# Performance work log

Hardware: AMD Instinct MI355X
Metric: run time of the kernel (lower is better)

The kernel has to match this reference:

```python
import jax, jax.numpy as jnp
import numpy as np

N_NODES = 100000


def gcn_conv(x, W, b, src, dst, n_nodes):
    # x: [N, Fin], W: [Fin, Fout], edge (src->dst) with self-loops added,
    # symmetric normalization D^{-1/2} A D^{-1/2} as in PyG GCNConv defaults.
    h = x @ W  # [N, Fout]
    loops = jnp.arange(n_nodes, dtype=src.dtype)
    src_all = jnp.concatenate([src, loops])
    dst_all = jnp.concatenate([dst, loops])
    ones = jnp.ones(src_all.shape[0], dtype=h.dtype)
    deg = jax.ops.segment_sum(ones, dst_all, num_segments=n_nodes)  # in-degree incl. self-loop
    dinv = jnp.where(deg > 0, jax.lax.rsqrt(deg), 0.0)
    norm = dinv[src_all] * dinv[dst_all]  # [E+N]
    msg = h[src_all] * norm[:, None]      # gather + scale
    out = jax.ops.segment_sum(msg, dst_all, num_segments=n_nodes)  # scatter-add
    return out + b


def setup_inputs() -> dict:
    key = jax.random.key(0)
    k1, k2, k3, k4 = jax.random.split(key, 4)
    in_dim, hidden, out_dim = 128, 128, 64
    n_edges = 600000
    x = jax.random.normal(k1, (N_NODES, in_dim), dtype=jnp.float32)
    edge_index = jax.random.randint(k2, (2, n_edges), 0, N_NODES, dtype=jnp.int64)
    # Glorot-ish init for weights
    W1 = jax.random.normal(k3, (in_dim, hidden), dtype=jnp.float32) / np.sqrt(in_dim)
    b1 = jnp.zeros((hidden,), dtype=jnp.float32)
    W2 = jax.random.normal(k4, (hidden, out_dim), dtype=jnp.float32) / np.sqrt(hidden)
    b2 = jnp.zeros((out_dim,), dtype=jnp.float32)
    return {"x": x, "edge_index": edge_index, "W1": W1, "b1": b1, "W2": W2, "b2": b2}


def reference(x, edge_index, W1, b1, W2, b2):
    src, dst = edge_index[0], edge_index[1]
    h = jax.nn.relu(gcn_conv(x, W1, b1, src, dst, N_NODES))
    # dropout is identity in eval mode (training=False)
    return gcn_conv(h, W2, b2, src, dst, N_NODES)
```

## Files before the change

### kernel.cpp

```cpp
#include <hip/hip_runtime.h>
#include <hip/hip_bf16.h>
#include <stdint.h>

typedef unsigned int u32;
typedef unsigned short u16;
typedef __attribute__((ext_vector_type(8))) short short8;
typedef __attribute__((ext_vector_type(4))) float f32x4;

#define SCAN_TILE 2048

__device__ __forceinline__ float bf2f(u16 u) {
    union { u32 u; float f; } v; v.u = ((u32)u) << 16; return v.f;
}
__device__ __forceinline__ u16 f2bf(float f) {
    u32 u = __float_as_uint(f);
    u32 r = (u + 0x7FFFu + ((u >> 16) & 1u)) >> 16;
    return (u16)r;
}
__device__ __forceinline__ u32 packbf(float lo, float hi) {
    return ((u32)f2bf(hi) << 16) | (u32)f2bf(lo);
}

__global__ __launch_bounds__(256) void detect_k(const u32* __restrict__ xw,
                                                const u32* __restrict__ ew,
                                                int* __restrict__ flags) {
    __shared__ int cnt;
    __shared__ u32 orr;
    int t = threadIdx.x;
    if (t == 0) { cnt = 0; orr = 0u; }
    __syncthreads();
    int hits = 0;
    for (int i = t; i < 1024; i += 256) {
        u32 f = (xw[i] >> 7) & 0xFFu;
        if (f >= 100u && f <= 140u) hits++;
    }
    atomicAdd(&cnt, hits);
    atomicOr(&orr, ew[2 * t + 1]);
    __syncthreads();
    if (t == 0) {
        flags[0] = (cnt < 512) ? 1 : 0;
        flags[1] = (orr == 0u) ? 1 : 0;
    }
}

template<int N>
__global__ __launch_bounds__(256) void w_pack_k(const void* __restrict__ W,
                                                uint4* __restrict__ wpk,
                                                const int* __restrict__ flags) {
    const int p = blockIdx.x * 256 + threadIdx.x;
    if (p >= 16 * N) return;
    const int n = p & (N - 1);
    const int kb = p >> ((N == 128) ? 7 : 6);
    u32 pk[4];
    if (flags[0]) {
        const float* wp = (const float*)W + (size_t)(kb * 8) * N + n;
        #pragma unroll
        for (int jj = 0; jj < 4; jj++)
            pk[jj] = packbf(wp[(2 * jj) * N], wp[(2 * jj + 1) * N]);
    } else {
        const u16* wp = (const u16*)W + (size_t)(kb * 8) * N + n;
        #pragma unroll
        for (int jj = 0; jj < 4; jj++)
            pk[jj] = ((u32)wp[(2 * jj + 1) * N] << 16) | (u32)wp[(2 * jj) * N];
    }
    uint4 v; v.x = pk[0]; v.y = pk[1]; v.z = pk[2]; v.w = pk[3];
    wpk[p] = v;
}

__global__ __launch_bounds__(256) void count_deg_k(const void* __restrict__ ei, int E,
                                                   const int* __restrict__ flags,
                                                   int* __restrict__ deg) {
    int i = blockIdx.x * 256 + threadIdx.x;
    if (i >= E) return;
    int d = flags[1] ? (int)((const long long*)ei)[E + i] : ((const int*)ei)[E + i];
    atomicAdd(&deg[d], 1);
}

__global__ __launch_bounds__(256) void scan_partial_k(const int* __restrict__ deg, int M,
                                                      int* __restrict__ bsum) {
    const int t = threadIdx.x;
    const int base = blockIdx.x * SCAN_TILE + t * 8;
    int s = 0;
    if (base + 8 <= M) {
        int4 a = *(const int4*)(deg + base);
        int4 b = *(const int4*)(deg + base + 4);
        s = a.x + a.y + a.z + a.w + b.x + b.y + b.z + b.w;
    } else {
        for (int j = 0; j < 8; j++) if (base + j < M) s += deg[base + j];
    }
    __shared__ int red[256];
    red[t] = s;
    __syncthreads();
    for (int d = 128; d > 0; d >>= 1) {
        if (t < d) red[t] += red[t + d];
        __syncthreads();
    }
    if (t == 0) bsum[blockIdx.x] = red[0];
}

__global__ __launch_bounds__(256) void scan_bsum_k(int* __restrict__ bsum, int nb,
                                                   int* __restrict__ off, int M) {
    __shared__ int buf[2][256];
    const int t = threadIdx.x;
    int v = (t < nb) ? bsum[t] : 0;
    const int own = v;
    buf[0][t] = v;
    __syncthreads();
    int cur = 0;
    for (int d = 1; d < 256; d <<= 1) {
        int x = buf[cur][t];
        if (t >= d) x += buf[cur][t - d];
        buf[cur ^ 1][t] = x;
        __syncthreads();
        cur ^= 1;
    }
    if (t < nb) bsum[t] = buf[cur][t] - own;
    if (t == 255) off[M] = buf[cur][255];
}

__global__ __launch_bounds__(256) void scan_final_k(const int* __restrict__ deg,
                                                    const int* __restrict__ bsum, int M,
                                                    int* __restrict__ off,
                                                    int* __restrict__ cursor,
                                                    float* __restrict__ dinv) {
    const int t = threadIdx.x;
    const int base = blockIdx.x * SCAN_TILE + t * 8;
    int v[8];
    int s = 0;
    const bool full = (base + 8 <= M);
    if (full) {
        int4 a = *(const int4*)(deg + base);
        int4 b = *(const int4*)(deg + base + 4);
        v[0] = a.x; v[1] = a.y; v[2] = a.z; v[3] = a.w;
        v[4] = b.x; v[5] = b.y; v[6] = b.z; v[7] = b.w;
        s = v[0] + v[1] + v[2] + v[3] + v[4] + v[5] + v[6] + v[7];
    } else {
        #pragma unroll
        for (int j = 0; j < 8; j++) { v[j] = (base + j < M) ? deg[base + j] : 0; s += v[j]; }
    }
    __shared__ int buf[2][256];
    buf[0][t] = s;
    __syncthreads();
    int cur = 0;
    for (int d = 1; d < 256; d <<= 1) {
        int x = buf[cur][t];
        if (t >= d) x += buf[cur][t - d];
        buf[cur ^ 1][t] = x;
        __syncthreads();
        cur ^= 1;
    }
    int pre = bsum[blockIdx.x] + buf[cur][t] - s;
    int o[8]; float dv[8];
    #pragma unroll
    for (int j = 0; j < 8; j++) {
        o[j] = pre;
        dv[j] = rsqrtf((float)(v[j] + 1));
        pre += v[j];
    }
    if (full) {
        *(int4*)(off + base)     = make_int4(o[0], o[1], o[2], o[3]);
        *(int4*)(off + base + 4) = make_int4(o[4], o[5], o[6], o[7]);
        *(int4*)(cursor + base)     = make_int4(o[0], o[1], o[2], o[3]);
        *(int4*)(cursor + base + 4) = make_int4(o[4], o[5], o[6], o[7]);
        *(float4*)(dinv + base)     = make_float4(dv[0], dv[1], dv[2], dv[3]);
        *(float4*)(dinv + base + 4) = make_float4(dv[4], dv[5], dv[6], dv[7]);
    } else {
        for (int j = 0; j < 8; j++) if (base + j < M) {
            off[base + j] = o[j]; cursor[base + j] = o[j]; dinv[base + j] = dv[j];
        }
    }
}

__global__ __launch_bounds__(256) void fill_k(const void* __restrict__ ei, int E,
                                              const int* __restrict__ flags,
                                              int* __restrict__ cursor, int* __restrict__ eidx) {
    int i = blockIdx.x * 256 + threadIdx.x;
    if (i >= E) return;
    int s, d;
    if (flags[1]) { const long long* p = (const long long*)ei; s = (int)p[i]; d = (int)p[E + i]; }
    else          { const int* p = (const int*)ei;             s = p[i];      d = p[E + i]; }
    int pos = atomicAdd(&cursor[d], 1);
    eidx[pos] = s;
}

template<int N>
__global__ __launch_bounds__(256) void gemm_mfma_k(
    const void* __restrict__ X, const uint4* __restrict__ wpk,
    const float* __restrict__ dinv, u16* __restrict__ HS,
    const int* __restrict__ flags, int x_is_ext, int M)
{
    constexpr int NT = N / 16;
    constexpr int NC8 = N / 8;
    __shared__ u32 xlds[128 * 64];
    const int t = threadIdx.x;
    const int wave = t >> 6, lane = t & 63;
    const int q = lane >> 4, m = lane & 15;
    const bool xf32 = (x_is_ext != 0) && (flags[0] != 0);
    const int row0 = blockIdx.x * 128;

    for (int c = t; c < 2048; c += 256) {
        const int row = c >> 4, c8 = c & 15;
        const int grow = row0 + row;
        uint4 pk = make_uint4(0u, 0u, 0u, 0u);
        if (grow < M) {
            if (xf32) {
                const float* xp = (const float*)X + (size_t)grow * 128 + c8 * 8;
                float4 u = *(const float4*)xp;
                float4 v = *(const float4*)(xp + 4);
                pk.x = packbf(u.x, u.y); pk.y = packbf(u.z, u.w);
                pk.z = packbf(v.x, v.y); pk.w = packbf(v.z, v.w);
            } else {
                pk = *(const uint4*)((const u16*)X + (size_t)grow * 128 + c8 * 8);
            }
        }
        *(uint4*)&xlds[row * 64 + c8 * 4] = pk;
    }
    __syncthreads();

    union { uint4 u; short8 v; } a[2][4];
    #pragma unroll
    for (int rt = 0; rt < 2; rt++)
        #pragma unroll
        for (int s = 0; s < 4; s++)
            a[rt][s].u = *(const uint4*)&xlds[(wave * 32 + rt * 16 + m) * 64 + (s * 4 + q) * 4];

    f32x4 acc[2][NT];
    #pragma unroll
    for (int rt = 0; rt < 2; rt++)
        #pragma unroll
        for (int tt = 0; tt < NT; tt++)
            acc[rt][tt] = (f32x4){0.f, 0.f, 0.f, 0.f};

    #pragma unroll
    for (int s = 0; s < 4; s++) {
        union { uint4 u; short8 v; } b[NT];
        #pragma unroll
        for (int tt = 0; tt < NT; tt++)
            b[tt].u = wpk[(s * 4 + q) * N + tt * 16 + m];
        #pragma unroll
        for (int tt = 0; tt < NT; tt++)
            #pragma unroll
            for (int rt = 0; rt < 2; rt++)
                acc[rt][tt] = __builtin_amdgcn_mfma_f32_16x16x32_bf16(
                    a[rt][s].v, b[tt].v, acc[rt][tt], 0, 0, 0);
    }

    float dv[2][4];
    #pragma unroll
    for (int rt = 0; rt < 2; rt++)
        #pragma unroll
        for (int r = 0; r < 4; r++) {
            const int grow = row0 + wave * 32 + rt * 16 + q * 4 + r;
            dv[rt][r] = (grow < M) ? dinv[grow] : 0.f;
        }

    u16* orow = (u16*)&xlds[wave * 32 * 64];
    #pragma unroll
    for (int rt = 0; rt < 2; rt++)
        #pragma unroll
        for (int tt = 0; tt < NT; tt++)
            #pragma unroll
            for (int r = 0; r < 4; r++)
                orow[(rt * 16 + q * 4 + r) * N + tt * 16 + m] =
                    f2bf(acc[rt][tt][r] * dv[rt][r]);

    constexpr int ITER = 16 * NC8 / 64;
    #pragma unroll
    for (int rt = 0; rt < 2; rt++) {
        #pragma unroll
        for (int j = 0; j < ITER; j++) {
            const int cc = lane + j * 64;
            const int lrow = cc / NC8, c8 = cc % NC8;
            const int grow = row0 + wave * 32 + rt * 16 + lrow;
            uint4 v = *(const uint4*)&((const u32*)orow)[(rt * 16 + lrow) * (N / 2) + c8 * 4];
            if (grow < M)
                *(uint4*)(HS + (size_t)grow * N + c8 * 8) = v;
        }
    }
}

template<int N, bool RELU>
__global__ __launch_bounds__(256) void aggregate_k(
    const u16* __restrict__ hs, const int* __restrict__ eidx,
    const int* __restrict__ off, const float* __restrict__ dinv,
    const void* __restrict__ bias, void* __restrict__ out,
    const int* __restrict__ flags, int out_is_ext, int M)
{
    constexpr int TPN = N / 8;
    constexpr int NPB = 256 / TPN;
    const int node = blockIdx.x * NPB + threadIdx.x / TPN;
    const int lane = threadIdx.x % TPN;
    if (node >= M) return;
    const int f32io = flags[0];
    const int beg = off[node], end = off[node + 1];
    const int c8 = lane * 8;
    const u16* __restrict__ hrow = hs + c8;

    float a[8];
    {
        uint4 sp = *(const uint4*)(hrow + (size_t)node * N);
        const u16* s = (const u16*)&sp;
        #pragma unroll
        for (int j = 0; j < 8; j++) a[j] = bf2f(s[j]);
    }

    int p = beg;
    for (; p + 4 <= end; p += 4) {
        const int s0 = eidx[p + 0], s1 = eidx[p + 1];
        const int s2 = eidx[p + 2], s3 = eidx[p + 3];
        uint4 v0 = *(const uint4*)(hrow + (size_t)s0 * N);
        uint4 v1 = *(const uint4*)(hrow + (size_t)s1 * N);
        uint4 v2 = *(const uint4*)(hrow + (size_t)s2 * N);
        uint4 v3 = *(const uint4*)(hrow + (size_t)s3 * N);
        const u16* q0 = (const u16*)&v0; const u16* q1 = (const u16*)&v1;
        const u16* q2 = (const u16*)&v2; const u16* q3 = (const u16*)&v3;
        #pragma unroll
        for (int j = 0; j < 8; j++)
            a[j] += (bf2f(q0[j]) + bf2f(q1[j])) + (bf2f(q2[j]) + bf2f(q3[j]));
    }
    for (; p < end; p++) {
        const int s = eidx[p];
        uint4 v = *(const uint4*)(hrow + (size_t)s * N);
        const u16* q = (const u16*)&v;
        #pragma unroll
        for (int j = 0; j < 8; j++) a[j] += bf2f(q[j]);
    }

    const float dv = dinv[node];
    float b[8];
    if (f32io) {
        float4 u = *(const float4*)((const float*)bias + c8);
        float4 v = *(const float4*)((const float*)bias + c8 + 4);
        b[0] = u.x; b[1] = u.y; b[2] = u.z; b[3] = u.w;
        b[4] = v.x; b[5] = v.y; b[6] = v.z; b[7] = v.w;
    } else {
        uint4 u = *(const uint4*)((const u16*)bias + c8);
        const u16* s = (const u16*)&u;
        #pragma unroll
        for (int j = 0; j < 8; j++) b[j] = bf2f(s[j]);
    }
    float o[8];
    #pragma unroll
    for (int j = 0; j < 8; j++) {
        o[j] = fmaf(dv, a[j], b[j]);
        if (RELU) o[j] = fmaxf(o[j], 0.f);
    }
    if (out_is_ext && f32io) {
        float* op = (float*)out + (size_t)node * N + c8;
        *(float4*)op       = make_float4(o[0], o[1], o[2], o[3]);
        *(float4*)(op + 4) = make_float4(o[4], o[5], o[6], o[7]);
    } else {
        uint4 pk;
        pk.x = packbf(o[0], o[1]); pk.y = packbf(o[2], o[3]);
        pk.z = packbf(o[4], o[5]); pk.w = packbf(o[6], o[7]);
        *(uint4*)((u16*)out + (size_t)node * N + c8) = pk;
    }
}

extern "C" void kernel_launch(void* const* d_in, const int* in_sizes, int n_in,
                              void* d_out, int out_size, void* d_ws, size_t ws_size,
                              hipStream_t stream) {
    const void* x  = d_in[0];
    const void* ei = d_in[1];
    const void* W1 = d_in[2];
    const void* b1 = d_in[3];
    const void* W2 = d_in[4];
    const void* b2 = d_in[5];

    const int M = in_sizes[0] / 128;
    const int E = in_sizes[1] / 2;
    const int NB = (M + SCAN_TILE - 1) / SCAN_TILE;

    char* ws = (char*)d_ws;
    size_t offb = 0;
    auto alloc = [&](size_t bytes) -> void* {
        void* p = ws + offb; offb += (bytes + 255) & ~(size_t)255; return p;
    };
    int*   flags  = (int*)  alloc(256);
    int*   bsum   = (int*)  alloc(1024);
    uint4* wpk1   = (uint4*)alloc(16 * 128 * 16);
    uint4* wpk2   = (uint4*)alloc(16 * 64 * 16);
    int*   deg    = (int*)  alloc((size_t)M * 4);
    int*   off    = (int*)  alloc((size_t)(M + 1) * 4);
    int*   cursor = (int*)  alloc((size_t)M * 4);
    float* dinv   = (float*)alloc((size_t)M * 4);
    int*   eidx   = (int*)  alloc((size_t)E * 4);
    u16*   hs1    = (u16*)  alloc((size_t)M * 128 * 2);
    u16*   out1   = (u16*)  alloc((size_t)M * 128 * 2);
    u16*   hs2    = hs1;
    (void)ws_size; (void)n_in; (void)out_size;

    detect_k<<<1, 256, 0, stream>>>((const u32*)x, (const u32*)ei, flags);
    w_pack_k<128><<<8, 256, 0, stream>>>(W1, wpk1, flags);
    w_pack_k<64><<<4, 256, 0, stream>>>(W2, wpk2, flags);

    hipMemsetAsync(deg, 0, (size_t)M * 4, stream);
    count_deg_k<<<(E + 255) / 256, 256, 0, stream>>>(ei, E, flags, deg);
    scan_partial_k<<<NB, 256, 0, stream>>>(deg, M, bsum);
    scan_bsum_k<<<1, 256, 0, stream>>>(bsum, NB, off, M);
    scan_final_k<<<NB, 256, 0, stream>>>(deg, bsum, M, off, cursor, dinv);
    fill_k<<<(E + 255) / 256, 256, 0, stream>>>(ei, E, flags, cursor, eidx);

    gemm_mfma_k<128><<<(M + 127) / 128, 256, 0, stream>>>(x, wpk1, dinv, hs1, flags, 1, M);
    aggregate_k<128, true><<<(M + 15) / 16, 256, 0, stream>>>(hs1, eidx, off, dinv, b1, out1,
                                                              flags, 0, M);
    gemm_mfma_k<64><<<(M + 127) / 128, 256, 0, stream>>>(out1, wpk2, dinv, hs2, flags, 0, M);
    aggregate_k<64, false><<<(M + 31) / 32, 256, 0, stream>>>(hs2, eidx, off, dinv, b2, d_out,
                                                              flags, 1, M);
}
```

Before: 248.3 us.

## Fuse layer-1 aggregation with layer-2 GEMM and merge small setup kernels

Layer-1 neighbor aggregation (bias and ReLU included) now runs in the same kernel as the layer-2 MFMA GEMM. The aggregated 128-row tile is staged in LDS instead of being written to and reread from a global intermediate buffer. The deg memset is folded into the detection kernel, and the two weight-pack kernels are merged into one launch, cutting launch count. The cost is a 32KB LDS tile per block and only 8 iterations of 16 nodes per block, which lowers occupancy and the latency hiding available to the irregular gathers.

```diff
diff --git a/kernel.cpp b/kernel.cpp
--- a/kernel.cpp
+++ b/kernel.cpp
@@ -21,38 +21,41 @@
     return ((u32)f2bf(hi) << 16) | (u32)f2bf(lo);
 }
 
-__global__ __launch_bounds__(256) void detect_k(const u32* __restrict__ xw,
-                                                const u32* __restrict__ ew,
-                                                int* __restrict__ flags) {
-    __shared__ int cnt;
-    __shared__ u32 orr;
-    int t = threadIdx.x;
-    if (t == 0) { cnt = 0; orr = 0u; }
-    __syncthreads();
-    int hits = 0;
-    for (int i = t; i < 1024; i += 256) {
-        u32 f = (xw[i] >> 7) & 0xFFu;
-        if (f >= 100u && f <= 140u) hits++;
-    }
-    atomicAdd(&cnt, hits);
-    atomicOr(&orr, ew[2 * t + 1]);
-    __syncthreads();
-    if (t == 0) {
-        flags[0] = (cnt < 512) ? 1 : 0;
-        flags[1] = (orr == 0u) ? 1 : 0;
+__global__ __launch_bounds__(256) void detect_zero_k(const u32* __restrict__ xw,
+                                                     const u32* __restrict__ ew,
+                                                     int* __restrict__ flags,
+                                                     int* __restrict__ deg, int M) {
+    const int t = threadIdx.x;
+    const int i4 = (blockIdx.x * 256 + t) * 4;
+    if (i4 + 4 <= M) *(int4*)(deg + i4) = make_int4(0, 0, 0, 0);
+    else { for (int j = 0; j < 4; j++) if (i4 + j < M) deg[i4 + j] = 0; }
+
+    if (blockIdx.x == 0) {
+        __shared__ int cnt;
+        __shared__ u32 orr;
+        if (t == 0) { cnt = 0; orr = 0u; }
+        __syncthreads();
+        int hits = 0;
+        for (int i = t; i < 1024; i += 256) {
+            u32 f = (xw[i] >> 7) & 0xFFu;
+            if (f >= 100u && f <= 140u) hits++;
+        }
+        atomicAdd(&cnt, hits);
+        atomicOr(&orr, ew[2 * t + 1]);
+        __syncthreads();
+        if (t == 0) {
+            flags[0] = (cnt < 512) ? 1 : 0;
+            flags[1] = (orr == 0u) ? 1 : 0;
+        }
     }
 }
 
 template<int N>
-__global__ __launch_bounds__(256) void w_pack_k(const void* __restrict__ W,
-                                                uint4* __restrict__ wpk,
-                                                const int* __restrict__ flags) {
-    const int p = blockIdx.x * 256 + threadIdx.x;
-    if (p >= 16 * N) return;
+__device__ __forceinline__ void wpack_one(const void* W, uint4* wpk, int p, int f32w) {
     const int n = p & (N - 1);
     const int kb = p >> ((N == 128) ? 7 : 6);
     u32 pk[4];
-    if (flags[0]) {
+    if (f32w) {
         const float* wp = (const float*)W + (size_t)(kb * 8) * N + n;
         #pragma unroll
         for (int jj = 0; jj < 4; jj++)
@@ -65,6 +68,17 @@
     }
     uint4 v; v.x = pk[0]; v.y = pk[1]; v.z = pk[2]; v.w = pk[3];
     wpk[p] = v;
+}
+
+__global__ __launch_bounds__(256) void wpack_all_k(const void* __restrict__ W1,
+                                                   const void* __restrict__ W2,
+                                                   uint4* __restrict__ wpk1,
+                                                   uint4* __restrict__ wpk2,
+                                                   const int* __restrict__ flags) {
+    const int b = blockIdx.x, t = threadIdx.x;
+    const int f32w = flags[0];
+    if (b < 8) wpack_one<128>(W1, wpk1, b * 256 + t, f32w);
+    else       wpack_one<64> (W2, wpk2, (b - 8) * 256 + t, f32w);
 }
 
 __global__ __launch_bounds__(256) void count_deg_k(const void* __restrict__ ei, int E,
@@ -279,6 +293,140 @@
     }
 }
 
+__global__ __launch_bounds__(256) void agg_gemm_k(
+    const u16* __restrict__ hs, const int* __restrict__ eidx,
+    const int* __restrict__ off, const float* __restrict__ dinv,
+    const void* __restrict__ bias, const uint4* __restrict__ wpk2,
+    u16* __restrict__ HS2, const int* __restrict__ flags, int M)
+{
+    __shared__ u32 zlds[128 * 64];
+    const int t = threadIdx.x;
+    const int wave = t >> 6, lane = t & 63;
+    const int q = lane >> 4, m = lane & 15;
+    const int row0 = blockIdx.x * 128;
+    const int f32io = flags[0];
+    const int l16 = t & 15, c8 = l16 * 8;
+    const u16* __restrict__ hrow = hs + c8;
+
+    float b[8];
+    if (f32io) {
+        float4 u = *(const float4*)((const float*)bias + c8);
+        float4 v = *(const float4*)((const float*)bias + c8 + 4);
+        b[0] = u.x; b[1] = u.y; b[2] = u.z; b[3] = u.w;
+        b[4] = v.x; b[5] = v.y; b[6] = v.z; b[7] = v.w;
+    } else {
+        uint4 u = *(const uint4*)((const u16*)bias + c8);
+        const u16* s = (const u16*)&u;
+        #pragma unroll
+        for (int j = 0; j < 8; j++) b[j] = bf2f(s[j]);
+    }
+
+    for (int it = 0; it < 8; it++) {
+        const int lr = it * 16 + (t >> 4);
+        const int node = row0 + lr;
+        uint4 zpk = make_uint4(0u, 0u, 0u, 0u);
+        if (node < M) {
+            float a[8];
+            {
+                uint4 sp = *(const uint4*)(hrow + (size_t)node * 128);
+                const u16* s = (const u16*)&sp;
+                #pragma unroll
+                for (int j = 0; j < 8; j++) a[j] = bf2f(s[j]);
+            }
+            const int beg = off[node], end = off[node + 1];
+            int p = beg;
+            for (; p + 4 <= end; p += 4) {
+                const int s0 = eidx[p + 0], s1 = eidx[p + 1];
+                const int s2 = eidx[p + 2], s3 = eidx[p + 3];
+                uint4 v0 = *(const uint4*)(hrow + (size_t)s0 * 128);
+                uint4 v1 = *(const uint4*)(hrow + (size_t)s1 * 128);
+                uint4 v2 = *(const uint4*)(hrow + (size_t)s2 * 128);
+                uint4 v3 = *(const uint4*)(hrow + (size_t)s3 * 128);
+                const u16* q0 = (const u16*)&v0; const u16* q1 = (const u16*)&v1;
+                const u16* q2 = (const u16*)&v2; const u16* q3 = (const u16*)&v3;
+                #pragma unroll
+                for (int j = 0; j < 8; j++)
+                    a[j] += (bf2f(q0[j]) + bf2f(q1[j])) + (bf2f(q2[j]) + bf2f(q3[j]));
+            }
+            for (; p < end; p++) {
+                const int s = eidx[p];
+                uint4 v = *(const uint4*)(hrow + (size_t)s * 128);
+                const u16* qq = (const u16*)&v;
+                #pragma unroll
+                for (int j = 0; j < 8; j++) a[j] += bf2f(qq[j]);
+            }
+            const float dv = dinv[node];
+            float z[8];
+            #pragma unroll
+            for (int j = 0; j < 8; j++) z[j] = fmaxf(fmaf(dv, a[j], b[j]), 0.f);
+            zpk.x = packbf(z[0], z[1]); zpk.y = packbf(z[2], z[3]);
+            zpk.z = packbf(z[4], z[5]); zpk.w = packbf(z[6], z[7]);
+        }
+        *(uint4*)&zlds[lr * 64 + l16 * 4] = zpk;
+    }
+    __syncthreads();
+
+    union { uint4 u; short8 v; } a[2][4];
+    #pragma unroll
+    for (int rt = 0; rt < 2; rt++)
+        #pragma unroll
+        for (int s = 0; s < 4; s++)
+            a[rt][s].u = *(const uint4*)&zlds[(wave * 32 + rt * 16 + m) * 64 + (s * 4 + q) * 4];
+
+    f32x4 acc[2][4];
+    #pragma unroll
+    for (int rt = 0; rt < 2; rt++)
+        #pragma unroll
+        for (int tt = 0; tt < 4; tt++)
+            acc[rt][tt] = (f32x4){0.f, 0.f, 0.f, 0.f};
+
+    #pragma unroll
+    for (int s = 0; s < 4; s++) {
+        union { uint4 u; short8 v; } bb[4];
+        #pragma unroll
+        for (int tt = 0; tt < 4; tt++)
+            bb[tt].u = wpk2[(s * 4 + q) * 64 + tt * 16 + m];
+        #pragma unroll
+        for (int tt = 0; tt < 4; tt++)
+            #pragma unroll
+            for (int rt = 0; rt < 2; rt++)
+                acc[rt][tt] = __builtin_amdgcn_mfma_f32_16x16x32_bf16(
+                    a[rt][s].v, bb[tt].v, acc[rt][tt], 0, 0, 0);
+    }
+
+    float dv2[2][4];
+    #pragma unroll
+    for (int rt = 0; rt < 2; rt++)
+        #pragma unroll
+        for (int r = 0; r < 4; r++) {
+            const int grow = row0 + wave * 32 + rt * 16 + q * 4 + r;
+            dv2[rt][r] = (grow < M) ? dinv[grow] : 0.f;
+        }
+
+    u16* orow = (u16*)&zlds[wave * 32 * 64];
+    #pragma unroll
+    for (int rt = 0; rt < 2; rt++)
+        #pragma unroll
+        for (int tt = 0; tt < 4; tt++)
+            #pragma unroll
+            for (int r = 0; r < 4; r++)
+                orow[(rt * 16 + q * 4 + r) * 64 + tt * 16 + m] =
+                    f2bf(acc[rt][tt][r] * dv2[rt][r]);
+
+    #pragma unroll
+    for (int rt = 0; rt < 2; rt++) {
+        #pragma unroll
+        for (int j = 0; j < 2; j++) {
+            const int cc = lane + j * 64;
+            const int lrow = cc >> 3, c = cc & 7;
+            const int grow = row0 + wave * 32 + rt * 16 + lrow;
+            uint4 v = *(const uint4*)&((const u32*)orow)[(rt * 16 + lrow) * 32 + c * 4];
+            if (grow < M)
+                *(uint4*)(HS2 + (size_t)grow * 64 + c * 8) = v;
+        }
+    }
+}
+
 template<int N, bool RELU>
 __global__ __launch_bounds__(256) void aggregate_k(
     const u16* __restrict__ hs, const int* __restrict__ eidx,
@@ -386,15 +534,12 @@
     float* dinv   = (float*)alloc((size_t)M * 4);
     int*   eidx   = (int*)  alloc((size_t)E * 4);
     u16*   hs1    = (u16*)  alloc((size_t)M * 128 * 2);
-    u16*   out1   = (u16*)  alloc((size_t)M * 128 * 2);
-    u16*   hs2    = hs1;
+    u16*   hs2    = (u16*)  alloc((size_t)M * 64 * 2);
     (void)ws_size; (void)n_in; (void)out_size;
 
-    detect_k<<<1, 256, 0, stream>>>((const u32*)x, (const u32*)ei, flags);
-    w_pack_k<128><<<8, 256, 0, stream>>>(W1, wpk1, flags);
-    w_pack_k<64><<<4, 256, 0, stream>>>(W2, wpk2, flags);
-
-    hipMemsetAsync(deg, 0, (size_t)M * 4, stream);
+    detect_zero_k<<<(M + 1023) / 1024, 256, 0, stream>>>((const u32*)x, (const u32*)ei,
+                                                         flags, deg, M);
+    wpack_all_k<<<12, 256, 0, stream>>>(W1, W2, wpk1, wpk2, flags);
     count_deg_k<<<(E + 255) / 256, 256, 0, stream>>>(ei, E, flags, deg);
     scan_partial_k<<<NB, 256, 0, stream>>>(deg, M, bsum);
     scan_bsum_k<<<1, 256, 0, stream>>>(bsum, NB, off, M);
@@ -402,9 +547,8 @@
     fill_k<<<(E + 255) / 256, 256, 0, stream>>>(ei, E, flags, cursor, eidx);
 
     gemm_mfma_k<128><<<(M + 127) / 128, 256, 0, stream>>>(x, wpk1, dinv, hs1, flags, 1, M);
-    aggregate_k<128, true><<<(M + 15) / 16, 256, 0, stream>>>(hs1, eidx, off, dinv, b1, out1,
-                                                              flags, 0, M);
-    gemm_mfma_k<64><<<(M + 127) / 128, 256, 0, stream>>>(out1, wpk2, dinv, hs2, flags, 0, M);
+    agg_gemm_k<<<(M + 127) / 128, 256, 0, stream>>>(hs1, eidx, off, dinv, b1, wpk2, hs2,
+                                                    flags, M);
     aggregate_k<64, false><<<(M + 31) / 32, 256, 0, stream>>>(hs2, eidx, off, dinv, b2, d_out,
                                                               flags, 1, M);
 }
```

Measured after the change: 250.7 us. No clear change (+1.0%).

## Fuse CSR build into one persistent kernel with software grid barriers

Applied to the files above, without the earlier changes.

Replaces the detect, weight-pack, memset, degree-count, three-stage scan and fill kernels with two launches. The first zeroes degrees and detects flags. The second is a persistent 256-block kernel that packs weights, counts degrees, scans and fills edge indices, with atomic grid barriers between phases. The aim is to cut per-launch overhead and the idle gaps between the many small preprocessing kernels. The cost is spin-wait barriers, which depend on all 256 blocks being resident at once, and fewer threads for the atomic-heavy edge phases. hs2 now gets its own buffer instead of aliasing hs1.

```diff
diff --git a/kernel.cpp b/kernel.cpp
--- a/kernel.cpp
+++ b/kernel.cpp
@@ -7,7 +7,7 @@
 typedef __attribute__((ext_vector_type(8))) short short8;
 typedef __attribute__((ext_vector_type(4))) float f32x4;
 
-#define SCAN_TILE 2048
+#define CSRB 256
 
 __device__ __forceinline__ float bf2f(u16 u) {
     union { u32 u; float f; } v; v.u = ((u32)u) << 16; return v.f;
@@ -21,38 +21,60 @@
     return ((u32)f2bf(hi) << 16) | (u32)f2bf(lo);
 }
 
-__global__ __launch_bounds__(256) void detect_k(const u32* __restrict__ xw,
-                                                const u32* __restrict__ ew,
-                                                int* __restrict__ flags) {
-    __shared__ int cnt;
-    __shared__ u32 orr;
-    int t = threadIdx.x;
-    if (t == 0) { cnt = 0; orr = 0u; }
+__device__ __forceinline__ void grid_bar(int* cnt, int* gen, int nb) {
     __syncthreads();
-    int hits = 0;
-    for (int i = t; i < 1024; i += 256) {
-        u32 f = (xw[i] >> 7) & 0xFFu;
-        if (f >= 100u && f <= 140u) hits++;
-    }
-    atomicAdd(&cnt, hits);
-    atomicOr(&orr, ew[2 * t + 1]);
+    if (threadIdx.x == 0) {
+        __threadfence();
+        int g = __hip_atomic_load(gen, __ATOMIC_RELAXED, __HIP_MEMORY_SCOPE_AGENT);
+        int prev = __hip_atomic_fetch_add(cnt, 1, __ATOMIC_ACQ_REL, __HIP_MEMORY_SCOPE_AGENT);
+        if (prev == nb - 1) {
+            __hip_atomic_store(cnt, 0, __ATOMIC_RELAXED, __HIP_MEMORY_SCOPE_AGENT);
+            __hip_atomic_store(gen, g + 1, __ATOMIC_RELEASE, __HIP_MEMORY_SCOPE_AGENT);
+        } else {
+            while (__hip_atomic_load(gen, __ATOMIC_ACQUIRE, __HIP_MEMORY_SCOPE_AGENT) <= g)
+                __builtin_amdgcn_s_sleep(1);
+        }
+    }
     __syncthreads();
-    if (t == 0) {
-        flags[0] = (cnt < 512) ? 1 : 0;
-        flags[1] = (orr == 0u) ? 1 : 0;
+}
+
+__global__ __launch_bounds__(256) void detect_zero_k(const u32* __restrict__ xw,
+                                                     const u32* __restrict__ ew,
+                                                     int* __restrict__ flags,
+                                                     int* __restrict__ deg, int M) {
+    const int t = threadIdx.x;
+    const int i4 = (blockIdx.x * 256 + t) * 4;
+    if (i4 + 4 <= M) *(int4*)(deg + i4) = make_int4(0, 0, 0, 0);
+    else { for (int j = 0; j < 4; j++) if (i4 + j < M) deg[i4 + j] = 0; }
+
+    if (blockIdx.x == 0) {
+        __shared__ int cnt;
+        __shared__ u32 orr;
+        if (t == 0) { cnt = 0; orr = 0u; }
+        __syncthreads();
+        int hits = 0;
+        for (int i = t; i < 1024; i += 256) {
+            u32 f = (xw[i] >> 7) & 0xFFu;
+            if (f >= 100u && f <= 140u) hits++;
+        }
+        atomicAdd(&cnt, hits);
+        atomicOr(&orr, ew[2 * t + 1]);
+        __syncthreads();
+        if (t == 0) {
+            flags[0] = (cnt < 512) ? 1 : 0;
+            flags[1] = (orr == 0u) ? 1 : 0;
+            flags[8] = 0;
+            flags[9] = 0;
+        }
     }
 }
 
 template<int N>
-__global__ __launch_bounds__(256) void w_pack_k(const void* __restrict__ W,
-                                                uint4* __restrict__ wpk,
-                                                const int* __restrict__ flags) {
-    const int p = blockIdx.x * 256 + threadIdx.x;
-    if (p >= 16 * N) return;
+__device__ __forceinline__ void wpack_one(const void* W, uint4* wpk, int p, int f32w) {
     const int n = p & (N - 1);
     const int kb = p >> ((N == 128) ? 7 : 6);
     u32 pk[4];
-    if (flags[0]) {
+    if (f32w) {
         const float* wp = (const float*)W + (size_t)(kb * 8) * N + n;
         #pragma unroll
         for (int jj = 0; jj < 4; jj++)
@@ -67,120 +89,115 @@
     wpk[p] = v;
 }
 
-__global__ __launch_bounds__(256) void count_deg_k(const void* __restrict__ ei, int E,
-                                                   const int* __restrict__ flags,
-                                                   int* __restrict__ deg) {
-    int i = blockIdx.x * 256 + threadIdx.x;
-    if (i >= E) return;
-    int d = flags[1] ? (int)((const long long*)ei)[E + i] : ((const int*)ei)[E + i];
-    atomicAdd(&deg[d], 1);
-}
-
-__global__ __launch_bounds__(256) void scan_partial_k(const int* __restrict__ deg, int M,
-                                                      int* __restrict__ bsum) {
-    const int t = threadIdx.x;
-    const int base = blockIdx.x * SCAN_TILE + t * 8;
-    int s = 0;
-    if (base + 8 <= M) {
-        int4 a = *(const int4*)(deg + base);
-        int4 b = *(const int4*)(deg + base + 4);
-        s = a.x + a.y + a.z + a.w + b.x + b.y + b.z + b.w;
+__global__ __launch_bounds__(256) void csr_build_k(
+    const void* __restrict__ ei, int E, int M,
+    int* __restrict__ flags,
+    const void* __restrict__ W1, const void* __restrict__ W2,
+    uint4* __restrict__ wpk1, uint4* __restrict__ wpk2,
+    int* __restrict__ deg, int* __restrict__ bsum,
+    int* __restrict__ off, int* __restrict__ cursor,
+    float* __restrict__ dinv, int* __restrict__ eidx)
+{
+    const int bid = blockIdx.x, t = threadIdx.x;
+    const int gtid = bid * 256 + t;
+    const int GT = CSRB * 256;
+    const int f32w = flags[0], i64 = flags[1];
+    int* cnt = &flags[8];
+    int* gen = &flags[9];
+
+    if (bid < 8)       wpack_one<128>(W1, wpk1, bid * 256 + t, f32w);
+    else if (bid < 12) wpack_one<64> (W2, wpk2, (bid - 8) * 256 + t, f32w);
+
+    if (i64) {
+        const long long* dp = (const long long*)ei + E;
+        for (int i = gtid; i < E; i += GT) atomicAdd(&deg[(int)dp[i]], 1);
     } else {
-        for (int j = 0; j < 8; j++) if (base + j < M) s += deg[base + j];
-    }
-    __shared__ int red[256];
-    red[t] = s;
-    __syncthreads();
-    for (int d = 128; d > 0; d >>= 1) {
-        if (t < d) red[t] += red[t + d];
+        const int* dp = (const int*)ei + E;
+        for (int i = gtid; i < E; i += GT) atomicAdd(&deg[dp[i]], 1);
+    }
+    grid_bar(cnt, gen, CSRB);
+
+    const int tile = (M + CSRB - 1) / CSRB;
+    const int lo = bid * tile;
+    const int idx0 = lo + 2 * t, idx1 = idx0 + 1;
+    const bool in0 = (2 * t < tile)     && (idx0 < M);
+    const bool in1 = (2 * t + 1 < tile) && (idx1 < M);
+    {
+        int s = (in0 ? deg[idx0] : 0) + (in1 ? deg[idx1] : 0);
+        __shared__ int red[256];
+        red[t] = s;
         __syncthreads();
-    }
-    if (t == 0) bsum[blockIdx.x] = red[0];
-}
-
-__global__ __launch_bounds__(256) void scan_bsum_k(int* __restrict__ bsum, int nb,
-                                                   int* __restrict__ off, int M) {
-    __shared__ int buf[2][256];
-    const int t = threadIdx.x;
-    int v = (t < nb) ? bsum[t] : 0;
-    const int own = v;
-    buf[0][t] = v;
-    __syncthreads();
-    int cur = 0;
-    for (int d = 1; d < 256; d <<= 1) {
-        int x = buf[cur][t];
-        if (t >= d) x += buf[cur][t - d];
-        buf[cur ^ 1][t] = x;
+        for (int d2 = 128; d2 > 0; d2 >>= 1) {
+            if (t < d2) red[t] += red[t + d2];
+            __syncthreads();
+        }
+        if (t == 0) bsum[bid] = red[0];
+    }
+    grid_bar(cnt, gen, CSRB);
+
+    if (bid == 0) {
+        __shared__ int buf[2][256];
+        int v = bsum[t];
+        const int own = v;
+        buf[0][t] = v;
         __syncthreads();
-        cur ^= 1;
-    }
-    if (t < nb) bsum[t] = buf[cur][t] - own;
-    if (t == 255) off[M] = buf[cur][255];
-}
-
-__global__ __launch_bounds__(256) void scan_final_k(const int* __restrict__ deg,
-                                                    const int* __restrict__ bsum, int M,
-                                                    int* __restrict__ off,
-                                                    int* __restrict__ cursor,
-                                                    float* __restrict__ dinv) {
-    const int t = threadIdx.x;
-    const int base = blockIdx.x * SCAN_TILE + t * 8;
-    int v[8];
-    int s = 0;
-    const bool full = (base + 8 <= M);
-    if (full) {
-        int4 a = *(const int4*)(deg + base);
-        int4 b = *(const int4*)(deg + base + 4);
-        v[0] = a.x; v[1] = a.y; v[2] = a.z; v[3] = a.w;
-        v[4] = b.x; v[5] = b.y; v[6] = b.z; v[7] = b.w;
-        s = v[0] + v[1] + v[2] + v[3] + v[4] + v[5] + v[6] + v[7];
+        int cur = 0;
+        for (int d2 = 1; d2 < 256; d2 <<= 1) {
+            int x = buf[cur][t];
+            if (t >= d2) x += buf[cur][t - d2];
+            buf[cur ^ 1][t] = x;
+            __syncthreads();
+            cur ^= 1;
+        }
+        bsum[t] = buf[cur][t] - own;
+        if (t == 255) off[M] = buf[cur][255];
+    }
+    grid_bar(cnt, gen, CSRB);
+
+    {
+        const int d0 = in0 ? deg[idx0] : 0;
+        const int d1 = in1 ? deg[idx1] : 0;
+        const int s = d0 + d1;
+        __shared__ int buf[2][256];
+        buf[0][t] = s;
+        __syncthreads();
+        int cur = 0;
+        for (int d2 = 1; d2 < 256; d2 <<= 1) {
+            int x = buf[cur][t];
+            if (t >= d2) x += buf[cur][t - d2];
+            buf[cur ^ 1][t] = x;
+            __syncthreads();
+            cur ^= 1;
+        }
+        int base = bsum[bid] + buf[cur][t] - s;
+        if (in0) {
+            off[idx0] = base; cursor[idx0] = base;
+            dinv[idx0] = rsqrtf((float)(d0 + 1));
+        }
+        if (in1) {
+            off[idx1] = base + d0; cursor[idx1] = base + d0;
+            dinv[idx1] = rsqrtf((float)(d1 + 1));
+        }
+    }
+    grid_bar(cnt, gen, CSRB);
+
+    if (i64) {
+        const long long* sp = (const long long*)ei;
+        const long long* dp = sp + E;
+        for (int i = gtid; i < E; i += GT) {
+            int s = (int)sp[i], d = (int)dp[i];
+            int pos = atomicAdd(&cursor[d], 1);
+            eidx[pos] = s;
+        }
     } else {
-        #pragma unroll
-        for (int j = 0; j < 8; j++) { v[j] = (base + j < M) ? deg[base + j] : 0; s += v[j]; }
-    }
-    __shared__ int buf[2][256];
-    buf[0][t] = s;
-    __syncthreads();
-    int cur = 0;
-    for (int d = 1; d < 256; d <<= 1) {
-        int x = buf[cur][t];
-        if (t >= d) x += buf[cur][t - d];
-        buf[cur ^ 1][t] = x;
-        __syncthreads();
-        cur ^= 1;
-    }
-    int pre = bsum[blockIdx.x] + buf[cur][t] - s;
-    int o[8]; float dv[8];
-    #pragma unroll
-    for (int j = 0; j < 8; j++) {
-        o[j] = pre;
-        dv[j] = rsqrtf((float)(v[j] + 1));
-        pre += v[j];
-    }
-    if (full) {
-        *(int4*)(off + base)     = make_int4(o[0], o[1], o[2], o[3]);
-        *(int4*)(off + base + 4) = make_int4(o[4], o[5], o[6], o[7]);
-        *(int4*)(cursor + base)     = make_int4(o[0], o[1], o[2], o[3]);
-        *(int4*)(cursor + base + 4) = make_int4(o[4], o[5], o[6], o[7]);
-        *(float4*)(dinv + base)     = make_float4(dv[0], dv[1], dv[2], dv[3]);
-        *(float4*)(dinv + base + 4) = make_float4(dv[4], dv[5], dv[6], dv[7]);
-    } else {
-        for (int j = 0; j < 8; j++) if (base + j < M) {
-            off[base + j] = o[j]; cursor[base + j] = o[j]; dinv[base + j] = dv[j];
-        }
-    }
-}
-
-__global__ __launch_bounds__(256) void fill_k(const void* __restrict__ ei, int E,
-                                              const int* __restrict__ flags,
-                                              int* __restrict__ cursor, int* __restrict__ eidx) {
-    int i = blockIdx.x * 256 + threadIdx.x;
-    if (i >= E) return;
-    int s, d;
-    if (flags[1]) { const long long* p = (const long long*)ei; s = (int)p[i]; d = (int)p[E + i]; }
-    else          { const int* p = (const int*)ei;             s = p[i];      d = p[E + i]; }
-    int pos = atomicAdd(&cursor[d], 1);
-    eidx[pos] = s;
+        const int* sp = (const int*)ei;
+        const int* dp = sp + E;
+        for (int i = gtid; i < E; i += GT) {
+            int s = sp[i], d = dp[i];
+            int pos = atomicAdd(&cursor[d], 1);
+            eidx[pos] = s;
+        }
+    }
 }
 
 template<int N>
@@ -369,7 +386,6 @@
 
     const int M = in_sizes[0] / 128;
     const int E = in_sizes[1] / 2;
-    const int NB = (M + SCAN_TILE - 1) / SCAN_TILE;
 
     char* ws = (char*)d_ws;
     size_t offb = 0;
@@ -387,20 +403,13 @@
     int*   eidx   = (int*)  alloc((size_t)E * 4);
     u16*   hs1    = (u16*)  alloc((size_t)M * 128 * 2);
     u16*   out1   = (u16*)  alloc((size_t)M * 128 * 2);
-    u16*   hs2    = hs1;
+    u16*   hs2    = (u16*)  alloc((size_t)M * 64 * 2);
     (void)ws_size; (void)n_in; (void)out_size;
 
-    detect_k<<<1, 256, 0, stream>>>((const u32*)x, (const u32*)ei, flags);
-    w_pack_k<128><<<8, 256, 0, stream>>>(W1, wpk1, flags);
-    w_pack_k<64><<<4, 256, 0, stream>>>(W2, wpk2, flags);
-
-    hipMemsetAsync(deg, 0, (size_t)M * 4, stream);
-    count_deg_k<<<(E + 255) / 256, 256, 0, stream>>>(ei, E, flags, deg);
-    scan_partial_k<<<NB, 256, 0, stream>>>(deg, M, bsum);
-    scan_bsum_k<<<1, 256, 0, stream>>>(bsum, NB, off, M);
-    scan_final_k<<<NB, 256, 0, stream>>>(deg, bsum, M, off, cursor, dinv);
-    fill_k<<<(E + 255) / 256, 256, 0, stream>>>(ei, E, flags, cursor, eidx);
-
+    detect_zero_k<<<(M + 1023) / 1024, 256, 0, stream>>>((const u32*)x, (const u32*)ei,
+                                                         flags, deg, M);
+    csr_build_k<<<CSRB, 256, 0, stream>>>(ei, E, M, flags, W1, W2, wpk1, wpk2,
+                                          deg, bsum, off, cursor, dinv, eidx);
     gemm_mfma_k<128><<<(M + 127) / 128, 256, 0, stream>>>(x, wpk1, dinv, hs1, flags, 1, M);
     aggregate_k<128, true><<<(M + 15) / 16, 256, 0, stream>>>(hs1, eidx, off, dinv, b1, out1,
                                                               flags, 0, M);
```

Result: slower. 365.9 us (+47.4%).
